# Kernel optimization log

Measured on AMD Instinct MI355X. Metric: run time of the kernel, lower is better.

## Reference

```python
import jax, jax.numpy as jnp
import numpy as np

NUM_FIELDS = 64
# itertools.combinations(range(n), 2) order == row-major upper-triangle (k=1)
_IU, _JU = np.triu_indices(NUM_FIELDS, k=1)
_IU = jnp.asarray(_IU)
_JU = jnp.asarray(_JU)


def setup_inputs() -> dict:
    key = jax.random.key(0)
    inputs = jax.random.normal(key, (16384, NUM_FIELDS, 32), dtype=jnp.float32)
    return {"inputs": inputs}


def reference(inputs) -> jnp.ndarray:
    # Gram matrix of field embeddings per sample: [B, F, F]
    gram = jnp.einsum("bfd,bgd->bfg", inputs, inputs)
    # Upper-triangle (i<j) pairs, same order as itertools.combinations: [B, F*(F-1)/2]
    return gram[:, _IU, _JU]
```

## Files before the change

kernel.cpp:

```cpp
#include <hip/hip_runtime.h>

#define NF 64
#define ND 32
#define NPAIR 2016

typedef __attribute__((ext_vector_type(8))) short bf16x8;
typedef __attribute__((ext_vector_type(4))) float f32x4;

__global__ __launch_bounds__(256, 5) void ip_gram_mfma(
    const float* __restrict__ in, float* __restrict__ out) {

    __shared__ float obuf[4][NPAIR];

    const int t = threadIdx.x;
    const int w = t >> 6;
    const int l = t & 63;
    const int s = blockIdx.x * 4 + w;

    const int q = l >> 4;
    const int m = l & 15;

    const float* src = in + (size_t)s * (NF * ND) + (q << 3);

    bf16x8 fhi[4], flo[4];
    #pragma unroll
    for (int r = 0; r < 4; ++r) {
        const float* rowp = src + (r * 16 + m) * ND;
        float4 v0 = ((const float4*)rowp)[0];
        float4 v1 = ((const float4*)rowp)[1];
        float xv[8] = {v0.x, v0.y, v0.z, v0.w, v1.x, v1.y, v1.z, v1.w};
        #pragma unroll
        for (int e = 0; e < 8; ++e) {
            unsigned xb = __builtin_bit_cast(unsigned, xv[e]);
            fhi[r][e] = (short)(xb >> 16);
            float hf = __builtin_bit_cast(float, xb & 0xFFFF0000u);
            float lf = xv[e] - hf;
            flo[r][e] = (short)(__builtin_bit_cast(unsigned, lf) >> 16);
        }
    }

    float* __restrict__ ob = obuf[w];
    #pragma unroll
    for (int ti = 0; ti < 4; ++ti) {
        #pragma unroll
        for (int tj = ti; tj < 4; ++tj) {
            f32x4 c = {0.f, 0.f, 0.f, 0.f};
            c = __builtin_amdgcn_mfma_f32_16x16x32_bf16(fhi[ti], fhi[tj], c, 0, 0, 0);
            c = __builtin_amdgcn_mfma_f32_16x16x32_bf16(fhi[ti], flo[tj], c, 0, 0, 0);
            c = __builtin_amdgcn_mfma_f32_16x16x32_bf16(flo[ti], fhi[tj], c, 0, 0, 0);
            int j = tj * 16 + m;
            #pragma unroll
            for (int r = 0; r < 4; ++r) {
                int i = ti * 16 + (q << 2) + r;
                if (ti < tj || j > i) {
                    int p = ((i * (127 - i)) >> 1) + j - i - 1;
                    ob[p] = c[r];
                }
            }
        }
    }

    float4* __restrict__ dst4 = (float4*)(out + (size_t)s * NPAIR);
    const float4* __restrict__ ob4 = (const float4*)ob;
    #pragma unroll
    for (int it = 0; it < 8; ++it) {
        int idx4 = l + (it << 6);
        if (idx4 < NPAIR / 4) {
            dst4[idx4] = ob4[idx4];
        }
    }
}

extern "C" void kernel_launch(void* const* d_in, const int* in_sizes, int n_in,
                              void* d_out, int out_size, void* d_ws, size_t ws_size,
                              hipStream_t stream) {
    const float* in = (const float*)d_in[0];
    float* out = (float*)d_out;
    const int nsamples = in_sizes[0] / (NF * ND);
    ip_gram_mfma<<<nsamples / 4, 256, 0, stream>>>(in, out);
}
```

Measured before the change: 231.8 us.

## Process four samples per wave with double-buffered register prefetch

Each wave now handles four consecutive samples instead of one. The next sample's input rows are loaded into a second register buffer while the current one is converted and multiplied. This hides global load latency behind MFMA and LDS work and amortizes launch overhead. In exchange the grid shrinks fourfold, there are more registers per thread (launch bounds lowered to 4 waves per SIMD), and fewer resident waves are available for latency hiding.

Result: slower. 237.9 us (+2.6%).

```diff
diff --git a/kernel.cpp b/kernel.cpp
--- a/kernel.cpp
+++ b/kernel.cpp
@@ -3,11 +3,12 @@
 #define NF 64
 #define ND 32
 #define NPAIR 2016
+#define SPW 4
 
 typedef __attribute__((ext_vector_type(8))) short bf16x8;
 typedef __attribute__((ext_vector_type(4))) float f32x4;
 
-__global__ __launch_bounds__(256, 5) void ip_gram_mfma(
+__global__ __launch_bounds__(256, 4) void ip_gram_mfma(
     const float* __restrict__ in, float* __restrict__ out) {
 
     __shared__ float obuf[4][NPAIR];
@@ -15,60 +16,80 @@
     const int t = threadIdx.x;
     const int w = t >> 6;
     const int l = t & 63;
-    const int s = blockIdx.x * 4 + w;
+    const int g = blockIdx.x * 4 + w;
+    const int s0 = g * SPW;
 
     const int q = l >> 4;
     const int m = l & 15;
 
-    const float* src = in + (size_t)s * (NF * ND) + (q << 3);
+    const float* src0 = in + (size_t)s0 * (NF * ND) + (q << 3);
+    float* __restrict__ ob = obuf[w];
 
-    bf16x8 fhi[4], flo[4];
-    #pragma unroll
-    for (int r = 0; r < 4; ++r) {
-        const float* rowp = src + (r * 16 + m) * ND;
-        float4 v0 = ((const float4*)rowp)[0];
-        float4 v1 = ((const float4*)rowp)[1];
-        float xv[8] = {v0.x, v0.y, v0.z, v0.w, v1.x, v1.y, v1.z, v1.w};
+    float4 bufA[8], bufB[8];
+
+    auto LOAD = [&](float4* buf, int k) {
+        const float* sp = src0 + k * (NF * ND);
         #pragma unroll
-        for (int e = 0; e < 8; ++e) {
-            unsigned xb = __builtin_bit_cast(unsigned, xv[e]);
-            fhi[r][e] = (short)(xb >> 16);
-            float hf = __builtin_bit_cast(float, xb & 0xFFFF0000u);
-            float lf = xv[e] - hf;
-            flo[r][e] = (short)(__builtin_bit_cast(unsigned, lf) >> 16);
+        for (int r = 0; r < 4; ++r) {
+            const float* rowp = sp + (r * 16 + m) * ND;
+            buf[2 * r]     = ((const float4*)rowp)[0];
+            buf[2 * r + 1] = ((const float4*)rowp)[1];
         }
-    }
+    };
 
-    float* __restrict__ ob = obuf[w];
-    #pragma unroll
-    for (int ti = 0; ti < 4; ++ti) {
+    auto PROCESS = [&](const float4* buf, int k) {
+        bf16x8 fhi[4], flo[4];
         #pragma unroll
-        for (int tj = ti; tj < 4; ++tj) {
-            f32x4 c = {0.f, 0.f, 0.f, 0.f};
-            c = __builtin_amdgcn_mfma_f32_16x16x32_bf16(fhi[ti], fhi[tj], c, 0, 0, 0);
-            c = __builtin_amdgcn_mfma_f32_16x16x32_bf16(fhi[ti], flo[tj], c, 0, 0, 0);
-            c = __builtin_amdgcn_mfma_f32_16x16x32_bf16(flo[ti], fhi[tj], c, 0, 0, 0);
-            int j = tj * 16 + m;
+        for (int r = 0; r < 4; ++r) {
+            float xv[8] = {buf[2*r].x, buf[2*r].y, buf[2*r].z, buf[2*r].w,
+                           buf[2*r+1].x, buf[2*r+1].y, buf[2*r+1].z, buf[2*r+1].w};
             #pragma unroll
-            for (int r = 0; r < 4; ++r) {
-                int i = ti * 16 + (q << 2) + r;
-                if (ti < tj || j > i) {
-                    int p = ((i * (127 - i)) >> 1) + j - i - 1;
-                    ob[p] = c[r];
+            for (int e = 0; e < 8; ++e) {
+                unsigned xb = __builtin_bit_cast(unsigned, xv[e]);
+                fhi[r][e] = (short)(xb >> 16);
+                float hf = __builtin_bit_cast(float, xb & 0xFFFF0000u);
+                float lf = xv[e] - hf;
+                flo[r][e] = (short)(__builtin_bit_cast(unsigned, lf) >> 16);
+            }
+        }
+        #pragma unroll
+        for (int ti = 0; ti < 4; ++ti) {
+            #pragma unroll
+            for (int tj = ti; tj < 4; ++tj) {
+                f32x4 c = {0.f, 0.f, 0.f, 0.f};
+                c = __builtin_amdgcn_mfma_f32_16x16x32_bf16(fhi[ti], fhi[tj], c, 0, 0, 0);
+                c = __builtin_amdgcn_mfma_f32_16x16x32_bf16(fhi[ti], flo[tj], c, 0, 0, 0);
+                c = __builtin_amdgcn_mfma_f32_16x16x32_bf16(flo[ti], fhi[tj], c, 0, 0, 0);
+                int j = tj * 16 + m;
+                #pragma unroll
+                for (int r = 0; r < 4; ++r) {
+                    int i = ti * 16 + (q << 2) + r;
+                    if (ti < tj || j > i) {
+                        int p = ((i * (127 - i)) >> 1) + j - i - 1;
+                        ob[p] = c[r];
+                    }
                 }
             }
         }
-    }
+        float4* __restrict__ dst4 = (float4*)(out + (size_t)(s0 + k) * NPAIR);
+        const float4* __restrict__ ob4 = (const float4*)ob;
+        #pragma unroll
+        for (int it = 0; it < 8; ++it) {
+            int idx4 = l + (it << 6);
+            if (idx4 < NPAIR / 4) {
+                dst4[idx4] = ob4[idx4];
+            }
+        }
+    };
 
-    float4* __restrict__ dst4 = (float4*)(out + (size_t)s * NPAIR);
-    const float4* __restrict__ ob4 = (const float4*)ob;
-    #pragma unroll
-    for (int it = 0; it < 8; ++it) {
-        int idx4 = l + (it << 6);
-        if (idx4 < NPAIR / 4) {
-            dst4[idx4] = ob4[idx4];
-        }
-    }
+    LOAD(bufA, 0);
+    LOAD(bufB, 1);
+    PROCESS(bufA, 0);
+    LOAD(bufA, 2);
+    PROCESS(bufB, 1);
+    LOAD(bufB, 3);
+    PROCESS(bufA, 2);
+    PROCESS(bufB, 3);
 }
 
 extern "C" void kernel_launch(void* const* d_in, const int* in_sizes, int n_in,
@@ -77,5 +98,5 @@
     const float* in = (const float*)d_in[0];
     float* out = (float*)d_out;
     const int nsamples = in_sizes[0] / (NF * ND);
-    ip_gram_mfma<<<nsamples / 4, 256, 0, stream>>>(in, out);
+    ip_gram_mfma<<<nsamples / (4 * SPW), 256, 0, stream>>>(in, out);
 }
```
